# Performance work log

Measured on AMD Instinct MI355X. Metric: run time of the kernel, lower is better.

## Reference

```python
import jax, jax.numpy as jnp
import numpy as np

N_NODES = 20000
N_EDGES = 640000
IN_F = 128
CL1_F = 128
CL2_F = 128
OUT_F = 2


def setup_inputs() -> dict:
    key = jax.random.key(0)
    ks = jax.random.split(key, 8)
    x = jax.random.normal(ks[0], (N_NODES, IN_F), dtype=jnp.float32)
    edge_index = jax.random.randint(ks[1], (2, N_EDGES), 0, N_NODES, dtype=jnp.int64)
    s1 = 1.0 / np.sqrt(IN_F)
    s2 = 1.0 / np.sqrt(CL1_F)
    s3 = 1.0 / np.sqrt(CL2_F)
    W1 = jax.random.uniform(ks[2], (IN_F, CL1_F), jnp.float32, -s1, s1)
    b1 = jax.random.uniform(ks[3], (CL1_F,), jnp.float32, -s1, s1)
    W2 = jax.random.uniform(ks[4], (CL1_F, CL2_F), jnp.float32, -s2, s2)
    b2 = jax.random.uniform(ks[5], (CL2_F,), jnp.float32, -s2, s2)
    W3 = jax.random.uniform(ks[6], (CL2_F, OUT_F), jnp.float32, -s3, s3)
    b3 = jax.random.uniform(ks[7], (OUT_F,), jnp.float32, -s3, s3)
    return {"x": x, "edge_index": edge_index, "W1": W1, "b1": b1,
            "W2": W2, "b2": b2, "W3": W3, "b3": b3}


def _scatter_mean(feat_src, src, dst, n_nodes):
    # out[i] = mean over edges e with dst[e]==i of feat_src gathered at src[e]
    msg = feat_src[src]                                   # [E, F] gather
    summed = jax.ops.segment_sum(msg, dst, num_segments=n_nodes)  # [N, F]
    ones = jnp.ones((src.shape[0],), dtype=feat_src.dtype)
    cnt = jax.ops.segment_sum(ones, dst, num_segments=n_nodes)    # [N]
    return summed / jnp.maximum(cnt, 1.0)[:, None]


def _mpnn_layer(x, src, dst, W, b, n_nodes):
    aggr = _scatter_mean(x, src, dst, n_nodes)
    return jax.nn.relu(aggr @ W + b)


def reference(x, edge_index, W1, b1, W2, b2, W3, b3):
    src, dst = edge_index[0], edge_index[1]
    n = x.shape[0]
    h = _mpnn_layer(x, src, dst, W1, b1, n)   # conv1 (update relu); extra relu is no-op
    h = _mpnn_layer(h, src, dst, W2, b2, n)   # conv2
    # dropout in eval mode is identity
    return h @ W3 + b3
```

## Files before the change

### kernel.cpp

```cpp
#include <hip/hip_runtime.h>

#define N_NODES 20000
#define N_EDGES 640000
#define F 128
#define CAP 128
#define ROWS 32


__global__ __launch_bounds__(256)
void bucket_kernel(const int* __restrict__ src, const int* __restrict__ dst,
                   int* __restrict__ cnt, int* __restrict__ bucket) {
    int e = blockIdx.x * blockDim.x + threadIdx.x;
    if (e >= N_EDGES) return;
    int d = dst[e];
    int pos = atomicAdd(&cnt[d], 1);
    if (pos < CAP) bucket[(size_t)d * CAP + pos] = src[e];
}

__global__ __launch_bounds__(256)
void fused_layer_kernel(const float* __restrict__ feat, const int* __restrict__ cnt,
                        const int* __restrict__ bucket, const float* __restrict__ W,
                        const float* __restrict__ b, float* __restrict__ out) {
    __shared__ float As[ROWS][F + 4];
    int tid  = threadIdx.x;
    int wave = tid >> 6;
    int lane = tid & 63;
    int half = lane >> 5;
    int sub  = lane & 31;
    int row0 = blockIdx.x * ROWS;

    const float4* f4 = (const float4*)feat;

    for (int t = 0; t < 8; ++t) {
        int nl   = wave * 8 + t;
        int node = row0 + nl;
        int deg  = cnt[node];
        const int* lst = bucket + (size_t)node * CAP;
        float4 acc; acc.x = acc.y = acc.z = acc.w = 0.f;
        int j = 0;
        for (; j + 16 <= deg; j += 16) {
            int4 ia = *(const int4*)(lst + j);
            int4 ib = *(const int4*)(lst + j + 4);
            int4 ic = *(const int4*)(lst + j + 8);
            int4 id = *(const int4*)(lst + j + 12);
            int i0 = half ? ia.y : ia.x;
            int i1 = half ? ia.w : ia.z;
            int i2 = half ? ib.y : ib.x;
            int i3 = half ? ib.w : ib.z;
            int i4 = half ? ic.y : ic.x;
            int i5 = half ? ic.w : ic.z;
            int i6 = half ? id.y : id.x;
            int i7 = half ? id.w : id.z;
            float4 v0 = f4[(size_t)i0 * 32 + sub];
            float4 v1 = f4[(size_t)i1 * 32 + sub];
            float4 v2 = f4[(size_t)i2 * 32 + sub];
            float4 v3 = f4[(size_t)i3 * 32 + sub];
            float4 v4 = f4[(size_t)i4 * 32 + sub];
            float4 v5 = f4[(size_t)i5 * 32 + sub];
            float4 v6 = f4[(size_t)i6 * 32 + sub];
            float4 v7 = f4[(size_t)i7 * 32 + sub];
            acc.x += ((v0.x + v1.x) + (v2.x + v3.x)) + ((v4.x + v5.x) + (v6.x + v7.x));
            acc.y += ((v0.y + v1.y) + (v2.y + v3.y)) + ((v4.y + v5.y) + (v6.y + v7.y));
            acc.z += ((v0.z + v1.z) + (v2.z + v3.z)) + ((v4.z + v5.z) + (v6.z + v7.z));
            acc.w += ((v0.w + v1.w) + (v2.w + v3.w)) + ((v4.w + v5.w) + (v6.w + v7.w));
        }
        for (; j + 2 <= deg; j += 2) {
            int2 ii = *(const int2*)(lst + j);
            int idx = half ? ii.y : ii.x;
            float4 v = f4[(size_t)idx * 32 + sub];
            acc.x += v.x; acc.y += v.y; acc.z += v.z; acc.w += v.w;
        }
        if (j < deg && half == 0) {
            float4 v = f4[(size_t)lst[j] * 32 + sub];
            acc.x += v.x; acc.y += v.y; acc.z += v.z; acc.w += v.w;
        }
        acc.x += __shfl(acc.x, lane ^ 32);
        acc.y += __shfl(acc.y, lane ^ 32);
        acc.z += __shfl(acc.z, lane ^ 32);
        acc.w += __shfl(acc.w, lane ^ 32);
        if (half == 0) {
            float inv = 1.0f / fmaxf((float)deg, 1.0f);
            float4 o; o.x = acc.x * inv; o.y = acc.y * inv; o.z = acc.z * inv; o.w = acc.w * inv;
            *(float4*)&As[nl][sub * 4] = o;
        }
    }
    __syncthreads();

    int tx = tid & 31, ty = tid >> 5;
    int c0 = tx * 4, r0 = ty * 4;
    float acc2[4][4] = {};

    for (int k = 0; k < F; k += 4) {
        float4 a4[4];
#pragma unroll
        for (int i = 0; i < 4; ++i) a4[i] = *(const float4*)&As[r0 + i][k];
#pragma unroll
        for (int u = 0; u < 4; ++u) {
            float4 w = *(const float4*)(W + (size_t)(k + u) * F + c0);
#pragma unroll
            for (int i = 0; i < 4; ++i) {
                float a = (u == 0) ? a4[i].x : (u == 1) ? a4[i].y : (u == 2) ? a4[i].z : a4[i].w;
                acc2[i][0] += a * w.x;
                acc2[i][1] += a * w.y;
                acc2[i][2] += a * w.z;
                acc2[i][3] += a * w.w;
            }
        }
    }

    float4 bias = *(const float4*)(b + c0);
#pragma unroll
    for (int i = 0; i < 4; ++i) {
        float4 o;
        o.x = fmaxf(acc2[i][0] + bias.x, 0.f);
        o.y = fmaxf(acc2[i][1] + bias.y, 0.f);
        o.z = fmaxf(acc2[i][2] + bias.z, 0.f);
        o.w = fmaxf(acc2[i][3] + bias.w, 0.f);
        *(float4*)(out + (size_t)(row0 + r0 + i) * F + c0) = o;
    }
}

__global__ __launch_bounds__(256)
void final_kernel(const float* __restrict__ h, const float* __restrict__ W3,
                  const float* __restrict__ b3, float* __restrict__ out) {
    int wid  = (blockIdx.x * blockDim.x + threadIdx.x) >> 6;
    int lane = threadIdx.x & 63;
    if (wid >= N_NODES) return;
    float2 v = ((const float2*)h)[(size_t)wid * 64 + lane];
    float4 w = ((const float4*)W3)[lane];
    float a0 = v.x * w.x + v.y * w.z;
    float a1 = v.x * w.y + v.y * w.w;
#pragma unroll
    for (int off = 32; off > 0; off >>= 1) {
        a0 += __shfl_down(a0, off);
        a1 += __shfl_down(a1, off);
    }
    if (lane == 0) {
        out[(size_t)wid * 2]     = a0 + b3[0];
        out[(size_t)wid * 2 + 1] = a1 + b3[1];
    }
}

extern "C" void kernel_launch(void* const* d_in, const int* in_sizes, int n_in,
                              void* d_out, int out_size, void* d_ws, size_t ws_size,
                              hipStream_t stream) {
    const float* x   = (const float*)d_in[0];
    const int*   ei  = (const int*)d_in[1];
    const int*   src = ei;
    const int*   dst = ei + N_EDGES;
    const float* W1 = (const float*)d_in[2];
    const float* b1 = (const float*)d_in[3];
    const float* W2 = (const float*)d_in[4];
    const float* b2 = (const float*)d_in[5];
    const float* W3 = (const float*)d_in[6];
    const float* b3 = (const float*)d_in[7];
    float* out = (float*)d_out;

    char* base = (char*)d_ws;
    size_t off = 0;
    auto take = [&](size_t bytes) -> char* {
        char* p = base + off;
        off += (bytes + 255) & ~(size_t)255;
        return p;
    };
    int*   cnt    = (int*)  take(N_NODES * sizeof(int));
    int*   bucket = (int*)  take((size_t)N_NODES * CAP * sizeof(int));
    float* h1     = (float*)take((size_t)N_NODES * F * sizeof(float));
    float* h2     = (float*)take((size_t)N_NODES * F * sizeof(float));

    hipMemsetAsync(cnt, 0, N_NODES * sizeof(int), stream);
    bucket_kernel<<<(N_EDGES + 255) / 256, 256, 0, stream>>>(src, dst, cnt, bucket);

    fused_layer_kernel<<<N_NODES / ROWS, 256, 0, stream>>>(x, cnt, bucket, W1, b1, h1);
    fused_layer_kernel<<<N_NODES / ROWS, 256, 0, stream>>>(h1, cnt, bucket, W2, b2, h2);
    final_kernel<<<(N_NODES * 64 + 255) / 256, 256, 0, stream>>>(h2, W3, b3, out);
}
```

Before: 227.0 us.

## Transform features before aggregation and fuse final projection into second aggregation

Result: faster. 215.2 us (-5.2%).

```diff
diff --git a/kernel.cpp b/kernel.cpp
--- a/kernel.cpp
+++ b/kernel.cpp
@@ -4,7 +4,6 @@
 #define N_EDGES 640000
 #define F 128
 #define CAP 128
-#define ROWS 32
 
 
 __global__ __launch_bounds__(256)
@@ -18,77 +17,23 @@
 }
 
 __global__ __launch_bounds__(256)
-void fused_layer_kernel(const float* __restrict__ feat, const int* __restrict__ cnt,
-                        const int* __restrict__ bucket, const float* __restrict__ W,
-                        const float* __restrict__ b, float* __restrict__ out) {
-    __shared__ float As[ROWS][F + 4];
+void gemm_kernel(const float* __restrict__ A, const float* __restrict__ W,
+                 float* __restrict__ C) {
+    __shared__ float As[32][F + 4];
     int tid  = threadIdx.x;
-    int wave = tid >> 6;
-    int lane = tid & 63;
-    int half = lane >> 5;
-    int sub  = lane & 31;
-    int row0 = blockIdx.x * ROWS;
-
-    const float4* f4 = (const float4*)feat;
-
-    for (int t = 0; t < 8; ++t) {
-        int nl   = wave * 8 + t;
-        int node = row0 + nl;
-        int deg  = cnt[node];
-        const int* lst = bucket + (size_t)node * CAP;
-        float4 acc; acc.x = acc.y = acc.z = acc.w = 0.f;
-        int j = 0;
-        for (; j + 16 <= deg; j += 16) {
-            int4 ia = *(const int4*)(lst + j);
-            int4 ib = *(const int4*)(lst + j + 4);
-            int4 ic = *(const int4*)(lst + j + 8);
-            int4 id = *(const int4*)(lst + j + 12);
-            int i0 = half ? ia.y : ia.x;
-            int i1 = half ? ia.w : ia.z;
-            int i2 = half ? ib.y : ib.x;
-            int i3 = half ? ib.w : ib.z;
-            int i4 = half ? ic.y : ic.x;
-            int i5 = half ? ic.w : ic.z;
-            int i6 = half ? id.y : id.x;
-            int i7 = half ? id.w : id.z;
-            float4 v0 = f4[(size_t)i0 * 32 + sub];
-            float4 v1 = f4[(size_t)i1 * 32 + sub];
-            float4 v2 = f4[(size_t)i2 * 32 + sub];
-            float4 v3 = f4[(size_t)i3 * 32 + sub];
-            float4 v4 = f4[(size_t)i4 * 32 + sub];
-            float4 v5 = f4[(size_t)i5 * 32 + sub];
-            float4 v6 = f4[(size_t)i6 * 32 + sub];
-            float4 v7 = f4[(size_t)i7 * 32 + sub];
-            acc.x += ((v0.x + v1.x) + (v2.x + v3.x)) + ((v4.x + v5.x) + (v6.x + v7.x));
-            acc.y += ((v0.y + v1.y) + (v2.y + v3.y)) + ((v4.y + v5.y) + (v6.y + v7.y));
-            acc.z += ((v0.z + v1.z) + (v2.z + v3.z)) + ((v4.z + v5.z) + (v6.z + v7.z));
-            acc.w += ((v0.w + v1.w) + (v2.w + v3.w)) + ((v4.w + v5.w) + (v6.w + v7.w));
-        }
-        for (; j + 2 <= deg; j += 2) {
-            int2 ii = *(const int2*)(lst + j);
-            int idx = half ? ii.y : ii.x;
-            float4 v = f4[(size_t)idx * 32 + sub];
-            acc.x += v.x; acc.y += v.y; acc.z += v.z; acc.w += v.w;
-        }
-        if (j < deg && half == 0) {
-            float4 v = f4[(size_t)lst[j] * 32 + sub];
-            acc.x += v.x; acc.y += v.y; acc.z += v.z; acc.w += v.w;
-        }
-        acc.x += __shfl(acc.x, lane ^ 32);
-        acc.y += __shfl(acc.y, lane ^ 32);
-        acc.z += __shfl(acc.z, lane ^ 32);
-        acc.w += __shfl(acc.w, lane ^ 32);
-        if (half == 0) {
-            float inv = 1.0f / fmaxf((float)deg, 1.0f);
-            float4 o; o.x = acc.x * inv; o.y = acc.y * inv; o.z = acc.z * inv; o.w = acc.w * inv;
-            *(float4*)&As[nl][sub * 4] = o;
-        }
+    int row0 = blockIdx.x * 32;
+
+    const float4* A4 = (const float4*)(A + (size_t)row0 * F);
+    for (int i = tid; i < 32 * 32; i += 256) {
+        float4 v = A4[i];
+        int r = i >> 5, c4 = (i & 31) * 4;
+        *(float4*)&As[r][c4] = v;
     }
     __syncthreads();
 
     int tx = tid & 31, ty = tid >> 5;
     int c0 = tx * 4, r0 = ty * 4;
-    float acc2[4][4] = {};
+    float acc[4][4] = {};
 
     for (int k = 0; k < F; k += 4) {
         float4 a4[4];
@@ -100,44 +45,167 @@
 #pragma unroll
             for (int i = 0; i < 4; ++i) {
                 float a = (u == 0) ? a4[i].x : (u == 1) ? a4[i].y : (u == 2) ? a4[i].z : a4[i].w;
-                acc2[i][0] += a * w.x;
-                acc2[i][1] += a * w.y;
-                acc2[i][2] += a * w.z;
-                acc2[i][3] += a * w.w;
+                acc[i][0] += a * w.x;
+                acc[i][1] += a * w.y;
+                acc[i][2] += a * w.z;
+                acc[i][3] += a * w.w;
             }
         }
     }
 
-    float4 bias = *(const float4*)(b + c0);
 #pragma unroll
     for (int i = 0; i < 4; ++i) {
         float4 o;
-        o.x = fmaxf(acc2[i][0] + bias.x, 0.f);
-        o.y = fmaxf(acc2[i][1] + bias.y, 0.f);
-        o.z = fmaxf(acc2[i][2] + bias.z, 0.f);
-        o.w = fmaxf(acc2[i][3] + bias.w, 0.f);
-        *(float4*)(out + (size_t)(row0 + r0 + i) * F + c0) = o;
-    }
-}
-
-__global__ __launch_bounds__(256)
-void final_kernel(const float* __restrict__ h, const float* __restrict__ W3,
-                  const float* __restrict__ b3, float* __restrict__ out) {
+        o.x = acc[i][0]; o.y = acc[i][1]; o.z = acc[i][2]; o.w = acc[i][3];
+        *(float4*)(C + (size_t)(row0 + r0 + i) * F + c0) = o;
+    }
+}
+
+__global__ __launch_bounds__(256)
+void agg_bias_relu_kernel(const float* __restrict__ y, const int* __restrict__ cnt,
+                          const int* __restrict__ bucket, const float* __restrict__ b,
+                          float* __restrict__ out) {
     int wid  = (blockIdx.x * blockDim.x + threadIdx.x) >> 6;
     int lane = threadIdx.x & 63;
     if (wid >= N_NODES) return;
-    float2 v = ((const float2*)h)[(size_t)wid * 64 + lane];
-    float4 w = ((const float4*)W3)[lane];
-    float a0 = v.x * w.x + v.y * w.z;
-    float a1 = v.x * w.y + v.y * w.w;
-#pragma unroll
-    for (int off = 32; off > 0; off >>= 1) {
-        a0 += __shfl_down(a0, off);
-        a1 += __shfl_down(a1, off);
+    int half = lane >> 5;
+    int sub  = lane & 31;
+    int deg  = cnt[wid];
+    const int* lst = bucket + (size_t)wid * CAP;
+    const float4* f4 = (const float4*)y;
+
+    float4 acc; acc.x = acc.y = acc.z = acc.w = 0.f;
+    int j = 0;
+    for (; j + 16 <= deg; j += 16) {
+        int4 ia = *(const int4*)(lst + j);
+        int4 ib = *(const int4*)(lst + j + 4);
+        int4 ic = *(const int4*)(lst + j + 8);
+        int4 id = *(const int4*)(lst + j + 12);
+        int i0 = half ? ia.y : ia.x;
+        int i1 = half ? ia.w : ia.z;
+        int i2 = half ? ib.y : ib.x;
+        int i3 = half ? ib.w : ib.z;
+        int i4 = half ? ic.y : ic.x;
+        int i5 = half ? ic.w : ic.z;
+        int i6 = half ? id.y : id.x;
+        int i7 = half ? id.w : id.z;
+        float4 v0 = f4[(size_t)i0 * 32 + sub];
+        float4 v1 = f4[(size_t)i1 * 32 + sub];
+        float4 v2 = f4[(size_t)i2 * 32 + sub];
+        float4 v3 = f4[(size_t)i3 * 32 + sub];
+        float4 v4 = f4[(size_t)i4 * 32 + sub];
+        float4 v5 = f4[(size_t)i5 * 32 + sub];
+        float4 v6 = f4[(size_t)i6 * 32 + sub];
+        float4 v7 = f4[(size_t)i7 * 32 + sub];
+        acc.x += ((v0.x + v1.x) + (v2.x + v3.x)) + ((v4.x + v5.x) + (v6.x + v7.x));
+        acc.y += ((v0.y + v1.y) + (v2.y + v3.y)) + ((v4.y + v5.y) + (v6.y + v7.y));
+        acc.z += ((v0.z + v1.z) + (v2.z + v3.z)) + ((v4.z + v5.z) + (v6.z + v7.z));
+        acc.w += ((v0.w + v1.w) + (v2.w + v3.w)) + ((v4.w + v5.w) + (v6.w + v7.w));
+    }
+    for (; j + 2 <= deg; j += 2) {
+        int2 ii = *(const int2*)(lst + j);
+        int idx = half ? ii.y : ii.x;
+        float4 v = f4[(size_t)idx * 32 + sub];
+        acc.x += v.x; acc.y += v.y; acc.z += v.z; acc.w += v.w;
+    }
+    if (j < deg && half == 0) {
+        float4 v = f4[(size_t)lst[j] * 32 + sub];
+        acc.x += v.x; acc.y += v.y; acc.z += v.z; acc.w += v.w;
+    }
+    acc.x += __shfl(acc.x, lane ^ 32);
+    acc.y += __shfl(acc.y, lane ^ 32);
+    acc.z += __shfl(acc.z, lane ^ 32);
+    acc.w += __shfl(acc.w, lane ^ 32);
+
+    if (half == 0) {
+        float inv = 1.0f / fmaxf((float)deg, 1.0f);
+        float4 bv = ((const float4*)b)[sub];
+        float4 o;
+        o.x = fmaxf(acc.x * inv + bv.x, 0.f);
+        o.y = fmaxf(acc.y * inv + bv.y, 0.f);
+        o.z = fmaxf(acc.z * inv + bv.z, 0.f);
+        o.w = fmaxf(acc.w * inv + bv.w, 0.f);
+        ((float4*)out)[(size_t)wid * 32 + sub] = o;
+    }
+}
+
+__global__ __launch_bounds__(256)
+void agg_final_kernel(const float* __restrict__ y, const int* __restrict__ cnt,
+                      const int* __restrict__ bucket, const float* __restrict__ b,
+                      const float* __restrict__ W3, const float* __restrict__ b3,
+                      float* __restrict__ out) {
+    int wid  = (blockIdx.x * blockDim.x + threadIdx.x) >> 6;
+    int lane = threadIdx.x & 63;
+    if (wid >= N_NODES) return;
+    int half = lane >> 5;
+    int sub  = lane & 31;
+    int deg  = cnt[wid];
+    const int* lst = bucket + (size_t)wid * CAP;
+    const float4* f4 = (const float4*)y;
+
+    float4 acc; acc.x = acc.y = acc.z = acc.w = 0.f;
+    int j = 0;
+    for (; j + 16 <= deg; j += 16) {
+        int4 ia = *(const int4*)(lst + j);
+        int4 ib = *(const int4*)(lst + j + 4);
+        int4 ic = *(const int4*)(lst + j + 8);
+        int4 id = *(const int4*)(lst + j + 12);
+        int i0 = half ? ia.y : ia.x;
+        int i1 = half ? ia.w : ia.z;
+        int i2 = half ? ib.y : ib.x;
+        int i3 = half ? ib.w : ib.z;
+        int i4 = half ? ic.y : ic.x;
+        int i5 = half ? ic.w : ic.z;
+        int i6 = half ? id.y : id.x;
+        int i7 = half ? id.w : id.z;
+        float4 v0 = f4[(size_t)i0 * 32 + sub];
+        float4 v1 = f4[(size_t)i1 * 32 + sub];
+        float4 v2 = f4[(size_t)i2 * 32 + sub];
+        float4 v3 = f4[(size_t)i3 * 32 + sub];
+        float4 v4 = f4[(size_t)i4 * 32 + sub];
+        float4 v5 = f4[(size_t)i5 * 32 + sub];
+        float4 v6 = f4[(size_t)i6 * 32 + sub];
+        float4 v7 = f4[(size_t)i7 * 32 + sub];
+        acc.x += ((v0.x + v1.x) + (v2.x + v3.x)) + ((v4.x + v5.x) + (v6.x + v7.x));
+        acc.y += ((v0.y + v1.y) + (v2.y + v3.y)) + ((v4.y + v5.y) + (v6.y + v7.y));
+        acc.z += ((v0.z + v1.z) + (v2.z + v3.z)) + ((v4.z + v5.z) + (v6.z + v7.z));
+        acc.w += ((v0.w + v1.w) + (v2.w + v3.w)) + ((v4.w + v5.w) + (v6.w + v7.w));
+    }
+    for (; j + 2 <= deg; j += 2) {
+        int2 ii = *(const int2*)(lst + j);
+        int idx = half ? ii.y : ii.x;
+        float4 v = f4[(size_t)idx * 32 + sub];
+        acc.x += v.x; acc.y += v.y; acc.z += v.z; acc.w += v.w;
+    }
+    if (j < deg && half == 0) {
+        float4 v = f4[(size_t)lst[j] * 32 + sub];
+        acc.x += v.x; acc.y += v.y; acc.z += v.z; acc.w += v.w;
+    }
+    acc.x += __shfl(acc.x, lane ^ 32);
+    acc.y += __shfl(acc.y, lane ^ 32);
+    acc.z += __shfl(acc.z, lane ^ 32);
+    acc.w += __shfl(acc.w, lane ^ 32);
+
+    float inv = 1.0f / fmaxf((float)deg, 1.0f);
+    float4 bv = ((const float4*)b)[sub];
+    float h0 = fmaxf(acc.x * inv + bv.x, 0.f);
+    float h1 = fmaxf(acc.y * inv + bv.y, 0.f);
+    float h2 = fmaxf(acc.z * inv + bv.z, 0.f);
+    float h3 = fmaxf(acc.w * inv + bv.w, 0.f);
+    float2 w0 = ((const float2*)W3)[sub * 4];
+    float2 w1 = ((const float2*)W3)[sub * 4 + 1];
+    float2 w2 = ((const float2*)W3)[sub * 4 + 2];
+    float2 w3 = ((const float2*)W3)[sub * 4 + 3];
+    float p0 = h0 * w0.x + h1 * w1.x + h2 * w2.x + h3 * w3.x;
+    float p1 = h0 * w0.y + h1 * w1.y + h2 * w2.y + h3 * w3.y;
+#pragma unroll
+    for (int off = 16; off > 0; off >>= 1) {
+        p0 += __shfl_down(p0, off, 32);
+        p1 += __shfl_down(p1, off, 32);
     }
     if (lane == 0) {
-        out[(size_t)wid * 2]     = a0 + b3[0];
-        out[(size_t)wid * 2 + 1] = a1 + b3[1];
+        float2 o; o.x = p0 + b3[0]; o.y = p1 + b3[1];
+        *(float2*)(out + (size_t)wid * 2) = o;
     }
 }
 
@@ -165,13 +233,14 @@
     };
     int*   cnt    = (int*)  take(N_NODES * sizeof(int));
     int*   bucket = (int*)  take((size_t)N_NODES * CAP * sizeof(int));
-    float* h1     = (float*)take((size_t)N_NODES * F * sizeof(float));
-    float* h2     = (float*)take((size_t)N_NODES * F * sizeof(float));
+    float* y      = (float*)take((size_t)N_NODES * F * sizeof(float));
+    float* h      = (float*)take((size_t)N_NODES * F * sizeof(float));
 
     hipMemsetAsync(cnt, 0, N_NODES * sizeof(int), stream);
     bucket_kernel<<<(N_EDGES + 255) / 256, 256, 0, stream>>>(src, dst, cnt, bucket);
 
-    fused_layer_kernel<<<N_NODES / ROWS, 256, 0, stream>>>(x, cnt, bucket, W1, b1, h1);
-    fused_layer_kernel<<<N_NODES / ROWS, 256, 0, stream>>>(h1, cnt, bucket, W2, b2, h2);
-    final_kernel<<<(N_NODES * 64 + 255) / 256, 256, 0, stream>>>(h2, W3, b3, out);
-}
+    gemm_kernel<<<N_NODES / 32, 256, 0, stream>>>(x, W1, y);
+    agg_bias_relu_kernel<<<(N_NODES * 64) / 256, 256, 0, stream>>>(y, cnt, bucket, b1, h);
+    gemm_kernel<<<N_NODES / 32, 256, 0, stream>>>(h, W2, y);
+    agg_final_kernel<<<(N_NODES * 64) / 256, 256, 0, stream>>>(y, cnt, bucket, b2, W3, b3, out);
+}
```
